# Performance work log

Hardware: AMD Instinct MI355X
Metric: run time of the kernel (lower is better)

## Reference

```python
import jax, jax.numpy as jnp
import numpy as np

B, S, E = 2, 2048, 2048
N_HEAD = 16
HEAD_DIM = E // N_HEAD  # 128
MP_NUM = 4              # hardcoded in the torch forward
ROTARY_DIM = 64


def setup_inputs() -> dict:
    key = jax.random.key(0)
    k1, k2, k3 = jax.random.split(key, 3)
    return {
        "hidden_states": jax.random.normal(k1, (B, S, E), jnp.float32) * 0.02,
        "w_qkv": jax.random.normal(k2, (3 * E, E), jnp.float32) * 0.02,  # torch Linear weight [out,in]
        "w_out": jax.random.normal(k3, (E, E), jnp.float32) * 0.02,
    }


def _rotate_every_two(x):
    # (..., d) -> interleaved (-x2, x1) as in GPT-J/CodeGen
    x1 = x[..., 0::2]
    x2 = x[..., 1::2]
    return jnp.stack((-x2, x1), axis=-1).reshape(x.shape)


def reference(hidden_states, w_qkv, w_out):
    b, s, e = hidden_states.shape
    local = e // MP_NUM  # per-mp-shard channel count

    # qkv projection (no bias), then mp_num split: order is (query, value, key)
    qkv = jnp.einsum("bse,fe->bsf", hidden_states, w_qkv)  # [B,S,3E]
    qkv = qkv.reshape(b, s, MP_NUM, 3 * local)
    q = qkv[..., :local].reshape(b, s, N_HEAD, HEAD_DIM)
    v = qkv[..., local:2 * local].reshape(b, s, N_HEAD, HEAD_DIM)
    k = qkv[..., 2 * local:].reshape(b, s, N_HEAD, HEAD_DIM)

    # partial rotary (rotate-every-two) on first ROTARY_DIM channels
    inv_freq = 1.0 / (10000.0 ** (jnp.arange(0, ROTARY_DIM, 2, dtype=jnp.float32) / ROTARY_DIM))
    freqs = jnp.arange(s, dtype=jnp.float32)[:, None] * inv_freq[None, :]  # [S, R/2]
    sin = jnp.repeat(jnp.sin(freqs), 2, axis=-1)[None, :, None, :]  # [1,S,1,R]
    cos = jnp.repeat(jnp.cos(freqs), 2, axis=-1)[None, :, None, :]

    def rope(x):
        x_rot = x[..., :ROTARY_DIM]
        x_pass = x[..., ROTARY_DIM:]
        x_rot = x_rot * cos + _rotate_every_two(x_rot) * sin
        return jnp.concatenate([x_rot, x_pass], axis=-1)

    q = rope(q)
    k = rope(k)

    # [B,S,H,D] -> [B,H,S,D]
    q = q.transpose(0, 2, 1, 3)
    k = k.transpose(0, 2, 1, 3)
    v = v.transpose(0, 2, 1, 3)

    scale = jnp.sqrt(jnp.asarray(HEAD_DIM, dtype=q.dtype))
    scores = jnp.einsum("bhqd,bhkd->bhqk", q, k) / scale  # [B,H,S,S]
    causal = jnp.tril(jnp.ones((s, s), dtype=bool))
    scores = jnp.where(causal[None, None, :, :], scores, jnp.finfo(scores.dtype).min)
    attn = jax.nn.softmax(scores, axis=-1)

    out = jnp.einsum("bhqk,bhkd->bhqd", attn, v)  # [B,H,S,D]
    out = out.transpose(0, 2, 1, 3).reshape(b, s, e)  # merge heads
    return jnp.einsum("bse,fe->bsf", out, w_out)  # out_proj (no bias)
```

## Files before the change

kernel.cpp:

```cpp
#include <hip/hip_runtime.h>

typedef unsigned short u16;
typedef unsigned int u32;
typedef __attribute__((ext_vector_type(4))) float f32x4;
typedef __attribute__((ext_vector_type(8))) short s16x8;
typedef __attribute__((ext_vector_type(4))) unsigned int u32x4;

#define DEVI static __device__ __forceinline__


#define ROPE_C (-13.287712379549449f / 32.0f)
#define QSCALE 0.12751743f

DEVI u16 f2bf(float f) {
  u32 u = __float_as_uint(f);
  return (u16)((u + 0x7FFFu + ((u >> 16) & 1u)) >> 16);
}
DEVI float bf2f(u16 h) { return __uint_as_float(((u32)h) << 16); }

DEVI void async_copy16(const u16* g, u16* l) {
  __builtin_amdgcn_global_load_lds((__attribute__((address_space(1))) void*)g,
                                   (__attribute__((address_space(3))) void*)l, 16, 0, 0);
}

__global__ __launch_bounds__(256) void cast3_kernel(
    const float* __restrict__ s0, u16* __restrict__ d0, int n0,
    const float* __restrict__ s1, u16* __restrict__ d1, int n1,
    const float* __restrict__ s2, u16* __restrict__ d2, int n2) {
  int i = blockIdx.x * 256 + threadIdx.x;
  const float* s;
  u16* d;
  if (i < n0) {
    s = s0; d = d0;
  } else if (i < n0 + n1) {
    s = s1; d = d1; i -= n0;
  } else if (i < n0 + n1 + n2) {
    s = s2; d = d2; i -= n0 + n1;
  } else {
    return;
  }
  const float4 v = ((const float4*)s)[i];
  ushort4 o;
  o.x = f2bf(v.x); o.y = f2bf(v.y); o.z = f2bf(v.z); o.w = f2bf(v.w);
  ((ushort4*)d)[i] = o;
}

template <int EPI>
__global__ __launch_bounds__(256, 3) void gemm_bt_kernel(
    const u16* __restrict__ A, const u16* __restrict__ Bm, int K, int N,
    float* __restrict__ C, u16* __restrict__ qo, u16* __restrict__ ko, u16* __restrict__ vo) {
  __shared__ __attribute__((aligned(16))) u16 As[3][128 * 32];
  __shared__ __attribute__((aligned(16))) u16 Bs[3][128 * 32];
  const int tid = threadIdx.x;
  const int w = tid >> 6, lane = tid & 63;
  const int quad = lane >> 4, l16 = lane & 15;
  const int wrow = (w >> 1) * 64, wcol = (w & 1) * 64;
  const long tileM = (long)blockIdx.y * 128;
  const long tileN = (long)blockIdx.x * 128;

  f32x4 acc[4][4];
#pragma unroll
  for (int i = 0; i < 4; ++i)
#pragma unroll
    for (int j = 0; j < 4; ++j) acc[i][j] = f32x4{0.f, 0.f, 0.f, 0.f};

  const u16* aptr[2];
  const u16* bptr[2];
  int ldso[2];
#pragma unroll
  for (int c = 0; c < 2; ++c) {
    const int r0 = (w * 2 + c) * 16;
    const int row = r0 + (lane >> 2);
    const int colsw = (((lane & 3) ^ ((row >> 1) & 3)) << 3);
    aptr[c] = A + (tileM + row) * (long)K + colsw;
    bptr[c] = Bm + (tileN + row) * (long)K + colsw;
    ldso[c] = r0 * 32;
  }

  auto stage = [&](int k0, int buf) {
#pragma unroll
    for (int c = 0; c < 2; ++c) {
      async_copy16(aptr[c] + k0, &As[buf][ldso[c]]);
      async_copy16(bptr[c] + k0, &Bs[buf][ldso[c]]);
    }
  };

  stage(0, 0);
  stage(32, 1);

  const int psw = (quad ^ ((l16 >> 1) & 3)) << 3;

  int bt = 0;
  for (int k0 = 0; k0 < K; k0 += 32) {
    if (k0 + 32 < K)
      __builtin_amdgcn_s_waitcnt(0x0f74);
    else
      __builtin_amdgcn_s_waitcnt(0x0f70);
    __builtin_amdgcn_s_barrier();
    if (k0 + 64 < K) stage(k0 + 64, bt == 0 ? 2 : bt - 1);

    s16x8 af[4], bfr[4];
#pragma unroll
    for (int i = 0; i < 4; ++i)
      af[i] = *(const s16x8*)(&As[bt][(wrow + i * 16 + l16) * 32 + psw]);
#pragma unroll
    for (int j = 0; j < 4; ++j)
      bfr[j] = *(const s16x8*)(&Bs[bt][(wcol + j * 16 + l16) * 32 + psw]);
#pragma unroll
    for (int i = 0; i < 4; ++i)
#pragma unroll
      for (int j = 0; j < 4; ++j)
        acc[i][j] = __builtin_amdgcn_mfma_f32_16x16x32_bf16(af[i], bfr[j], acc[i][j], 0, 0, 0);
    bt = bt == 2 ? 0 : bt + 1;
  }

  const int b = (int)(tileM >> 11);
#pragma unroll
  for (int i = 0; i < 4; ++i) {
#pragma unroll
    for (int j = 0; j < 4; ++j) {
      const int rowb = (int)((tileM + wrow + i * 16 + quad * 4) & 2047);
      if (EPI == 0) {
#pragma unroll
        for (int r = 0; r < 4; ++r) {
          const long row = tileM + wrow + i * 16 + quad * 4 + r;
          C[row * N + tileN + wcol + j * 16 + l16] = acc[i][j][r];
        }
      } else {
        const long col0 = tileN + wcol + j * 16;
        const int mp = (int)(col0 / 1536);
        const int cc0 = (int)(col0 - (long)mp * 1536);
        const int part = cc0 >> 9;
        const int idx0 = cc0 & 511;
        const int head = mp * 4 + (idx0 >> 7);
        const int dim0 = idx0 & 127;
        const int dim = dim0 + l16;
        const long bh = (long)(b * 16 + head);
        if (part == 1) {
#pragma unroll
          for (int r = 0; r < 4; ++r)
            vo[(bh * 128 + dim) * 2048 + rowb + r] = f2bf(acc[i][j][r]);
        } else {
          float y[4];
          if (part == 2 && dim0 < 64) {
            const int jj = dim >> 1;
            const float inv = exp2f((float)jj * ROPE_C);
#pragma unroll
            for (int r = 0; r < 4; ++r) {
              const float v = acc[i][j][r];
              const float pv = __shfl_xor(v, 1, 64);
              const float ang = (float)(rowb + r) * inv;
              const float sn = __sinf(ang), cs = __cosf(ang);
              y[r] = (l16 & 1) ? (v * cs + pv * sn) : (v * cs - pv * sn);
            }
          } else {
#pragma unroll
            for (int r = 0; r < 4; ++r) y[r] = acc[i][j][r];
          }
          u16* dst = (part == 0) ? qo : ko;
#pragma unroll
          for (int r = 0; r < 4; ++r)
            dst[(bh * 2048 + rowb + r) * 128 + dim] = f2bf(y[r]);
        }
      }
    }
  }
}

__global__ __launch_bounds__(256, 3) void attn_kernel(
    const u16* __restrict__ q, const u16* __restrict__ k,
    const u16* __restrict__ vT, u16* __restrict__ out) {
  __shared__ __attribute__((aligned(16))) u16 Ks[3][32 * 128];
  __shared__ __attribute__((aligned(16))) u16 Vs[3][128 * 32];
  const int tid = threadIdx.x;
  const int w = tid >> 6, lane = tid & 63;
  const int quad = lane >> 4, l16 = lane & 15;
  const int qt = 31 - (blockIdx.x >> 5);
  const int bh = blockIdx.x & 31;
  const int qbase = qt * 64 + w * 16;

  const u16* qp = q + ((long)bh * 2048 + qbase) * 128;
  const u16* kp = k + (long)bh * 2048 * 128;
  const u16* vp = vT + (long)bh * 128 * 2048;

  const float spos = (float)(qbase + l16);
  s16x8 qf[4];
#pragma unroll
  for (int c = 0; c < 4; ++c) {
    const s16x8 raw = *(const s16x8*)(qp + l16 * 128 + c * 32 + quad * 8);
    s16x8 ov;
    if (c < 2) {
#pragma unroll
      for (int m = 0; m < 4; ++m) {
        const int jj = c * 16 + quad * 4 + m;
        const float inv = exp2f((float)jj * ROPE_C);
        const float ang = spos * inv;
        const float sn = __sinf(ang), cs = __cosf(ang);
        const float x0 = bf2f((u16)raw[2 * m]), x1 = bf2f((u16)raw[2 * m + 1]);
        ov[2 * m] = (short)f2bf((x0 * cs - x1 * sn) * QSCALE);
        ov[2 * m + 1] = (short)f2bf((x1 * cs + x0 * sn) * QSCALE);
      }
    } else {
#pragma unroll
      for (int e = 0; e < 8; ++e) ov[e] = (short)f2bf(bf2f((u16)raw[e]) * QSCALE);
    }
    qf[c] = ov;
  }

  f32x4 acc[8];
#pragma unroll
  for (int d = 0; d < 8; ++d) acc[d] = f32x4{0.f, 0.f, 0.f, 0.f};
  float mrun = -1e30f, lrun = 0.f;

  auto stage = [&](int k0, int buf) {
    const int ko = lane >> 4, cl = lane & 15;
#pragma unroll
    for (int i = 0; i < 2; ++i) {
      const int keyt = w * 8 + i * 4;
      const int rr = keyt + ko;
      const int sk = ((rr >> 2) & 3) * 8 + ((rr >> 4) & 1) * 4 + (rr & 3);
      async_copy16(kp + (long)(k0 + sk) * 128 + ((cl ^ (rr & 15)) << 3),
                   &Ks[buf][keyt * 128]);
    }
    const int ld = lane >> 2, c4 = lane & 3;
#pragma unroll
    for (int i = 0; i < 2; ++i) {
      const int db = w * 32 + i * 16;
      const int d = db + ld;
      async_copy16(vp + (long)d * 2048 + k0 + ((c4 ^ ((d >> 1) & 3)) << 3),
                   &Vs[buf][db * 32]);
    }
  };

  const int nt = 2 * qt + 2;
  stage(0, 0);
  stage(32, 1);

  int bt = 0;
  for (int t = 0; t < nt; ++t) {
    const int k0 = t * 32;
    if (t + 1 < nt)
      __builtin_amdgcn_s_waitcnt(0x0f74);
    else
      __builtin_amdgcn_s_waitcnt(0x0f70);
    __builtin_amdgcn_s_barrier();
    if (t + 2 < nt) stage(k0 + 64, bt == 0 ? 2 : bt - 1);
    const u16* Ksc = Ks[bt];
    const u16* Vsc = Vs[bt];

    f32x4 sc[2];
    sc[0] = f32x4{0.f, 0.f, 0.f, 0.f};
    sc[1] = f32x4{0.f, 0.f, 0.f, 0.f};
    __builtin_amdgcn_s_setprio(1);
#pragma unroll
    for (int c = 0; c < 4; ++c) {
      const s16x8 kf0 = *(const s16x8*)(
          &Ksc[(0 * 16 + l16) * 128 + ((((c << 2) + quad) ^ l16) << 3)]);
      const s16x8 kf1 = *(const s16x8*)(
          &Ksc[(1 * 16 + l16) * 128 + ((((c << 2) + quad) ^ l16) << 3)]);
      sc[0] = __builtin_amdgcn_mfma_f32_16x16x32_bf16(kf0, qf[c], sc[0], 0, 0, 0);
      sc[1] = __builtin_amdgcn_mfma_f32_16x16x32_bf16(kf1, qf[c], sc[1], 0, 0, 0);
    }
    __builtin_amdgcn_s_setprio(0);
    if (k0 + 31 > qbase) {
      const int qrow = qbase + l16;
#pragma unroll
      for (int g = 0; g < 2; ++g) {
        const int keyb = k0 + quad * 8 + g * 4;
#pragma unroll
        for (int r = 0; r < 4; ++r)
          if (keyb + r > qrow) sc[g][r] = -1e30f;
      }
    }
    float mx = fmaxf(fmaxf(fmaxf(sc[0][0], sc[0][1]), fmaxf(sc[0][2], sc[0][3])),
                     fmaxf(fmaxf(sc[1][0], sc[1][1]), fmaxf(sc[1][2], sc[1][3])));
    mx = fmaxf(mx, __shfl_xor(mx, 16, 64));
    mx = fmaxf(mx, __shfl_xor(mx, 32, 64));
    if (__any(mx > mrun + 8.f)) {
      const float mnew = fmaxf(mrun, mx);
      const float alpha = exp2f(mrun - mnew);
      mrun = mnew;
      lrun *= alpha;
#pragma unroll
      for (int d = 0; d < 8; ++d)
#pragma unroll
        for (int r = 0; r < 4; ++r) acc[d][r] *= alpha;
    }
    float p[2][4];
    float sm = 0.f;
#pragma unroll
    for (int g = 0; g < 2; ++g)
#pragma unroll
      for (int r = 0; r < 4; ++r) { p[g][r] = exp2f(sc[g][r] - mrun); sm += p[g][r]; }
    sm += __shfl_xor(sm, 16, 64);
    sm += __shfl_xor(sm, 32, 64);
    lrun += sm;

    u32 pk[2][2];
#pragma unroll
    for (int g = 0; g < 2; ++g) {
      pk[g][0] = (u32)f2bf(p[g][0]) | ((u32)f2bf(p[g][1]) << 16);
      pk[g][1] = (u32)f2bf(p[g][2]) | ((u32)f2bf(p[g][3]) << 16);
    }
    const u32x4 pw = {pk[0][0], pk[0][1], pk[1][0], pk[1][1]};
    const s16x8 pf = __builtin_bit_cast(s16x8, pw);

    __builtin_amdgcn_s_setprio(1);
#pragma unroll
    for (int dd = 0; dd < 8; ++dd) {
      const s16x8 vf = *(const s16x8*)(
          &Vsc[(dd * 16 + l16) * 32 + ((quad ^ ((l16 >> 1) & 3)) << 3)]);
      acc[dd] = __builtin_amdgcn_mfma_f32_16x16x32_bf16(vf, pf, acc[dd], 0, 0, 0);
    }
    __builtin_amdgcn_s_setprio(0);
    bt = bt == 2 ? 0 : bt + 1;
  }

  const int b = bh >> 4, h = bh & 15;
  u16* op = out + ((long)b * 2048 + qbase + l16) * 2048 + h * 128;
  const float inv_l = 1.0f / lrun;
#pragma unroll
  for (int dd = 0; dd < 8; ++dd) {
    ushort4 o4;
    o4.x = f2bf(acc[dd][0] * inv_l);
    o4.y = f2bf(acc[dd][1] * inv_l);
    o4.z = f2bf(acc[dd][2] * inv_l);
    o4.w = f2bf(acc[dd][3] * inv_l);
    *(ushort4*)(op + dd * 16 + quad * 4) = o4;
  }
}

extern "C" void kernel_launch(void* const* d_in, const int* in_sizes, int n_in,
                              void* d_out, int out_size, void* d_ws, size_t ws_size,
                              hipStream_t stream) {
  const float* hidden = (const float*)d_in[0];
  const float* w_qkv = (const float*)d_in[1];
  const float* w_out = (const float*)d_in[2];
  float* out = (float*)d_out;
  char* ws = (char*)d_ws;

  u16* hid_b  = (u16*)(ws + (size_t)0);
  u16* wqkv_b = (u16*)(ws + (size_t)16777216);
  u16* wout_b = (u16*)(ws + (size_t)41943040);
  u16* qb     = (u16*)(ws + (size_t)50331648);
  u16* kb     = (u16*)(ws + (size_t)67108864);
  u16* vb     = (u16*)(ws + (size_t)83886080);
  u16* ao     = (u16*)(ws + (size_t)100663296);

  cast3_kernel<<<24576, 256, 0, stream>>>(hidden, hid_b, 2097152,
                                          w_qkv, wqkv_b, 3145728,
                                          w_out, wout_b, 1048576);

  gemm_bt_kernel<1><<<dim3(48, 32), 256, 0, stream>>>(hid_b, wqkv_b, 2048, 6144,
                                                      nullptr, qb, kb, vb);
  attn_kernel<<<1024, 256, 0, stream>>>(qb, kb, vb, ao);
  gemm_bt_kernel<0><<<dim3(16, 32), 256, 0, stream>>>(ao, wout_b, 2048, 2048,
                                                      out, nullptr, nullptr, nullptr);
}
```

Baseline: 373.9 us.

## Process two query groups per attention block to reuse staged K/V tiles

```diff
diff --git a/kernel.cpp b/kernel.cpp
--- a/kernel.cpp
+++ b/kernel.cpp
@@ -167,7 +167,7 @@
   }
 }
 
-__global__ __launch_bounds__(256, 3) void attn_kernel(
+__global__ __launch_bounds__(256, 2) void attn_kernel(
     const u16* __restrict__ q, const u16* __restrict__ k,
     const u16* __restrict__ vT, u16* __restrict__ out) {
   __shared__ __attribute__((aligned(16))) u16 Ks[3][32 * 128];
@@ -175,42 +175,50 @@
   const int tid = threadIdx.x;
   const int w = tid >> 6, lane = tid & 63;
   const int quad = lane >> 4, l16 = lane & 15;
-  const int qt = 31 - (blockIdx.x >> 5);
+  const int qt = 15 - (blockIdx.x >> 5);
   const int bh = blockIdx.x & 31;
-  const int qbase = qt * 64 + w * 16;
-
-  const u16* qp = q + ((long)bh * 2048 + qbase) * 128;
+  const int qb0 = qt * 128 + w * 16;
+  const int qb1 = qb0 + 64;
+
+  const u16* qp = q + ((long)bh * 2048 + qb0) * 128;
   const u16* kp = k + (long)bh * 2048 * 128;
   const u16* vp = vT + (long)bh * 128 * 2048;
 
-  const float spos = (float)(qbase + l16);
-  s16x8 qf[4];
-#pragma unroll
-  for (int c = 0; c < 4; ++c) {
-    const s16x8 raw = *(const s16x8*)(qp + l16 * 128 + c * 32 + quad * 8);
-    s16x8 ov;
-    if (c < 2) {
-#pragma unroll
-      for (int m = 0; m < 4; ++m) {
-        const int jj = c * 16 + quad * 4 + m;
-        const float inv = exp2f((float)jj * ROPE_C);
-        const float ang = spos * inv;
-        const float sn = __sinf(ang), cs = __cosf(ang);
-        const float x0 = bf2f((u16)raw[2 * m]), x1 = bf2f((u16)raw[2 * m + 1]);
-        ov[2 * m] = (short)f2bf((x0 * cs - x1 * sn) * QSCALE);
-        ov[2 * m + 1] = (short)f2bf((x1 * cs + x0 * sn) * QSCALE);
-      }
-    } else {
-#pragma unroll
-      for (int e = 0; e < 8; ++e) ov[e] = (short)f2bf(bf2f((u16)raw[e]) * QSCALE);
-    }
-    qf[c] = ov;
-  }
-
-  f32x4 acc[8];
-#pragma unroll
-  for (int d = 0; d < 8; ++d) acc[d] = f32x4{0.f, 0.f, 0.f, 0.f};
-  float mrun = -1e30f, lrun = 0.f;
+  s16x8 qf[2][4];
+#pragma unroll
+  for (int qg = 0; qg < 2; ++qg) {
+    const float spos = (float)((qg ? qb1 : qb0) + l16);
+    const u16* qpg = qp + (qg ? 64 * 128 : 0);
+#pragma unroll
+    for (int c = 0; c < 4; ++c) {
+      const s16x8 raw = *(const s16x8*)(qpg + l16 * 128 + c * 32 + quad * 8);
+      s16x8 ov;
+      if (c < 2) {
+#pragma unroll
+        for (int m = 0; m < 4; ++m) {
+          const int jj = c * 16 + quad * 4 + m;
+          const float inv = exp2f((float)jj * ROPE_C);
+          const float ang = spos * inv;
+          const float sn = __sinf(ang), cs = __cosf(ang);
+          const float x0 = bf2f((u16)raw[2 * m]), x1 = bf2f((u16)raw[2 * m + 1]);
+          ov[2 * m] = (short)f2bf((x0 * cs - x1 * sn) * QSCALE);
+          ov[2 * m + 1] = (short)f2bf((x1 * cs + x0 * sn) * QSCALE);
+        }
+      } else {
+#pragma unroll
+        for (int e = 0; e < 8; ++e) ov[e] = (short)f2bf(bf2f((u16)raw[e]) * QSCALE);
+      }
+      qf[qg][c] = ov;
+    }
+  }
+
+  f32x4 acc[2][8];
+#pragma unroll
+  for (int qg = 0; qg < 2; ++qg)
+#pragma unroll
+    for (int d = 0; d < 8; ++d) acc[qg][d] = f32x4{0.f, 0.f, 0.f, 0.f};
+  float mrun0 = -1e30f, lrun0 = 0.f;
+  float mrun1 = -1e30f, lrun1 = 0.f;
 
   auto stage = [&](int k0, int buf) {
     const int ko = lane >> 4, cl = lane & 15;
@@ -232,7 +240,7 @@
     }
   };
 
-  const int nt = 2 * qt + 2;
+  const int nt = 4 * qt + 4;
   stage(0, 0);
   stage(32, 1);
 
@@ -247,10 +255,17 @@
     if (t + 2 < nt) stage(k0 + 64, bt == 0 ? 2 : bt - 1);
     const u16* Ksc = Ks[bt];
     const u16* Vsc = Vs[bt];
-
-    f32x4 sc[2];
-    sc[0] = f32x4{0.f, 0.f, 0.f, 0.f};
-    sc[1] = f32x4{0.f, 0.f, 0.f, 0.f};
+    bt = bt == 2 ? 0 : bt + 1;
+
+    const bool act1 = (k0 <= qb1 + 15);
+    const bool act0 = (k0 <= qb0 + 15);
+    if (!act1) continue;
+
+    f32x4 sc0[2], sc1[2];
+    sc0[0] = f32x4{0.f, 0.f, 0.f, 0.f};
+    sc0[1] = f32x4{0.f, 0.f, 0.f, 0.f};
+    sc1[0] = f32x4{0.f, 0.f, 0.f, 0.f};
+    sc1[1] = f32x4{0.f, 0.f, 0.f, 0.f};
     __builtin_amdgcn_s_setprio(1);
 #pragma unroll
     for (int c = 0; c < 4; ++c) {
@@ -258,75 +273,128 @@
           &Ksc[(0 * 16 + l16) * 128 + ((((c << 2) + quad) ^ l16) << 3)]);
       const s16x8 kf1 = *(const s16x8*)(
           &Ksc[(1 * 16 + l16) * 128 + ((((c << 2) + quad) ^ l16) << 3)]);
-      sc[0] = __builtin_amdgcn_mfma_f32_16x16x32_bf16(kf0, qf[c], sc[0], 0, 0, 0);
-      sc[1] = __builtin_amdgcn_mfma_f32_16x16x32_bf16(kf1, qf[c], sc[1], 0, 0, 0);
+      if (act0) {
+        sc0[0] = __builtin_amdgcn_mfma_f32_16x16x32_bf16(kf0, qf[0][c], sc0[0], 0, 0, 0);
+        sc0[1] = __builtin_amdgcn_mfma_f32_16x16x32_bf16(kf1, qf[0][c], sc0[1], 0, 0, 0);
+      }
+      sc1[0] = __builtin_amdgcn_mfma_f32_16x16x32_bf16(kf0, qf[1][c], sc1[0], 0, 0, 0);
+      sc1[1] = __builtin_amdgcn_mfma_f32_16x16x32_bf16(kf1, qf[1][c], sc1[1], 0, 0, 0);
     }
     __builtin_amdgcn_s_setprio(0);
-    if (k0 + 31 > qbase) {
-      const int qrow = qbase + l16;
+
+    if (k0 + 31 > qb1) {
+      const int qrow = qb1 + l16;
 #pragma unroll
       for (int g = 0; g < 2; ++g) {
         const int keyb = k0 + quad * 8 + g * 4;
 #pragma unroll
         for (int r = 0; r < 4; ++r)
-          if (keyb + r > qrow) sc[g][r] = -1e30f;
-      }
-    }
-    float mx = fmaxf(fmaxf(fmaxf(sc[0][0], sc[0][1]), fmaxf(sc[0][2], sc[0][3])),
-                     fmaxf(fmaxf(sc[1][0], sc[1][1]), fmaxf(sc[1][2], sc[1][3])));
-    mx = fmaxf(mx, __shfl_xor(mx, 16, 64));
-    mx = fmaxf(mx, __shfl_xor(mx, 32, 64));
-    if (__any(mx > mrun + 8.f)) {
-      const float mnew = fmaxf(mrun, mx);
-      const float alpha = exp2f(mrun - mnew);
-      mrun = mnew;
-      lrun *= alpha;
+          if (keyb + r > qrow) sc1[g][r] = -1e30f;
+      }
+    }
+    float mx1 = fmaxf(fmaxf(fmaxf(sc1[0][0], sc1[0][1]), fmaxf(sc1[0][2], sc1[0][3])),
+                      fmaxf(fmaxf(sc1[1][0], sc1[1][1]), fmaxf(sc1[1][2], sc1[1][3])));
+    mx1 = fmaxf(mx1, __shfl_xor(mx1, 16, 64));
+    mx1 = fmaxf(mx1, __shfl_xor(mx1, 32, 64));
+    if (__any(mx1 > mrun1 + 8.f)) {
+      const float mnew = fmaxf(mrun1, mx1);
+      const float alpha = exp2f(mrun1 - mnew);
+      mrun1 = mnew;
+      lrun1 *= alpha;
 #pragma unroll
       for (int d = 0; d < 8; ++d)
 #pragma unroll
-        for (int r = 0; r < 4; ++r) acc[d][r] *= alpha;
-    }
-    float p[2][4];
-    float sm = 0.f;
+        for (int r = 0; r < 4; ++r) acc[1][d][r] *= alpha;
+    }
+    float p1[2][4];
+    float sm1 = 0.f;
 #pragma unroll
     for (int g = 0; g < 2; ++g)
 #pragma unroll
-      for (int r = 0; r < 4; ++r) { p[g][r] = exp2f(sc[g][r] - mrun); sm += p[g][r]; }
-    sm += __shfl_xor(sm, 16, 64);
-    sm += __shfl_xor(sm, 32, 64);
-    lrun += sm;
-
-    u32 pk[2][2];
+      for (int r = 0; r < 4; ++r) { p1[g][r] = exp2f(sc1[g][r] - mrun1); sm1 += p1[g][r]; }
+    sm1 += __shfl_xor(sm1, 16, 64);
+    sm1 += __shfl_xor(sm1, 32, 64);
+    lrun1 += sm1;
+    u32 pk1[2][2];
 #pragma unroll
     for (int g = 0; g < 2; ++g) {
-      pk[g][0] = (u32)f2bf(p[g][0]) | ((u32)f2bf(p[g][1]) << 16);
-      pk[g][1] = (u32)f2bf(p[g][2]) | ((u32)f2bf(p[g][3]) << 16);
-    }
-    const u32x4 pw = {pk[0][0], pk[0][1], pk[1][0], pk[1][1]};
-    const s16x8 pf = __builtin_bit_cast(s16x8, pw);
+      pk1[g][0] = (u32)f2bf(p1[g][0]) | ((u32)f2bf(p1[g][1]) << 16);
+      pk1[g][1] = (u32)f2bf(p1[g][2]) | ((u32)f2bf(p1[g][3]) << 16);
+    }
+    const u32x4 pw1 = {pk1[0][0], pk1[0][1], pk1[1][0], pk1[1][1]};
+    const s16x8 pf1 = __builtin_bit_cast(s16x8, pw1);
+
+    s16x8 pf0;
+    if (act0) {
+      if (k0 + 31 > qb0) {
+        const int qrow = qb0 + l16;
+#pragma unroll
+        for (int g = 0; g < 2; ++g) {
+          const int keyb = k0 + quad * 8 + g * 4;
+#pragma unroll
+          for (int r = 0; r < 4; ++r)
+            if (keyb + r > qrow) sc0[g][r] = -1e30f;
+        }
+      }
+      float mx0 = fmaxf(fmaxf(fmaxf(sc0[0][0], sc0[0][1]), fmaxf(sc0[0][2], sc0[0][3])),
+                        fmaxf(fmaxf(sc0[1][0], sc0[1][1]), fmaxf(sc0[1][2], sc0[1][3])));
+      mx0 = fmaxf(mx0, __shfl_xor(mx0, 16, 64));
+      mx0 = fmaxf(mx0, __shfl_xor(mx0, 32, 64));
+      if (__any(mx0 > mrun0 + 8.f)) {
+        const float mnew = fmaxf(mrun0, mx0);
+        const float alpha = exp2f(mrun0 - mnew);
+        mrun0 = mnew;
+        lrun0 *= alpha;
+#pragma unroll
+        for (int d = 0; d < 8; ++d)
+#pragma unroll
+          for (int r = 0; r < 4; ++r) acc[0][d][r] *= alpha;
+      }
+      float p0[2][4];
+      float sm0 = 0.f;
+#pragma unroll
+      for (int g = 0; g < 2; ++g)
+#pragma unroll
+        for (int r = 0; r < 4; ++r) { p0[g][r] = exp2f(sc0[g][r] - mrun0); sm0 += p0[g][r]; }
+      sm0 += __shfl_xor(sm0, 16, 64);
+      sm0 += __shfl_xor(sm0, 32, 64);
+      lrun0 += sm0;
+      u32 pk0[2][2];
+#pragma unroll
+      for (int g = 0; g < 2; ++g) {
+        pk0[g][0] = (u32)f2bf(p0[g][0]) | ((u32)f2bf(p0[g][1]) << 16);
+        pk0[g][1] = (u32)f2bf(p0[g][2]) | ((u32)f2bf(p0[g][3]) << 16);
+      }
+      const u32x4 pw0 = {pk0[0][0], pk0[0][1], pk0[1][0], pk0[1][1]};
+      pf0 = __builtin_bit_cast(s16x8, pw0);
+    }
 
     __builtin_amdgcn_s_setprio(1);
 #pragma unroll
     for (int dd = 0; dd < 8; ++dd) {
       const s16x8 vf = *(const s16x8*)(
           &Vsc[(dd * 16 + l16) * 32 + ((quad ^ ((l16 >> 1) & 3)) << 3)]);
-      acc[dd] = __builtin_amdgcn_mfma_f32_16x16x32_bf16(vf, pf, acc[dd], 0, 0, 0);
+      if (act0)
+        acc[0][dd] = __builtin_amdgcn_mfma_f32_16x16x32_bf16(vf, pf0, acc[0][dd], 0, 0, 0);
+      acc[1][dd] = __builtin_amdgcn_mfma_f32_16x16x32_bf16(vf, pf1, acc[1][dd], 0, 0, 0);
     }
     __builtin_amdgcn_s_setprio(0);
-    bt = bt == 2 ? 0 : bt + 1;
   }
 
   const int b = bh >> 4, h = bh & 15;
-  u16* op = out + ((long)b * 2048 + qbase + l16) * 2048 + h * 128;
-  const float inv_l = 1.0f / lrun;
-#pragma unroll
-  for (int dd = 0; dd < 8; ++dd) {
-    ushort4 o4;
-    o4.x = f2bf(acc[dd][0] * inv_l);
-    o4.y = f2bf(acc[dd][1] * inv_l);
-    o4.z = f2bf(acc[dd][2] * inv_l);
-    o4.w = f2bf(acc[dd][3] * inv_l);
-    *(ushort4*)(op + dd * 16 + quad * 4) = o4;
+#pragma unroll
+  for (int qg = 0; qg < 2; ++qg) {
+    u16* op = out + ((long)b * 2048 + (qg ? qb1 : qb0) + l16) * 2048 + h * 128;
+    const float inv_l = 1.0f / (qg ? lrun1 : lrun0);
+#pragma unroll
+    for (int dd = 0; dd < 8; ++dd) {
+      ushort4 o4;
+      o4.x = f2bf(acc[qg][dd][0] * inv_l);
+      o4.y = f2bf(acc[qg][dd][1] * inv_l);
+      o4.z = f2bf(acc[qg][dd][2] * inv_l);
+      o4.w = f2bf(acc[qg][dd][3] * inv_l);
+      *(ushort4*)(op + dd * 16 + quad * 4) = o4;
+    }
   }
 }
 
@@ -353,7 +421,7 @@
 
   gemm_bt_kernel<1><<<dim3(48, 32), 256, 0, stream>>>(hid_b, wqkv_b, 2048, 6144,
                                                       nullptr, qb, kb, vb);
-  attn_kernel<<<1024, 256, 0, stream>>>(qb, kb, vb, ao);
+  attn_kernel<<<512, 256, 0, stream>>>(qb, kb, vb, ao);
   gemm_bt_kernel<0><<<dim3(16, 32), 256, 0, stream>>>(ao, wout_b, 2048, 2048,
                                                       out, nullptr, nullptr, nullptr);
 }
```

Measured after the change: 417.0 us. 1.12x slower.

## Switch attention to 32x32x16 MFMA with 2-wave blocks and double buffering

Applied to the files above, without the earlier changes.

```diff
diff --git a/kernel.cpp b/kernel.cpp
--- a/kernel.cpp
+++ b/kernel.cpp
@@ -3,6 +3,7 @@
 typedef unsigned short u16;
 typedef unsigned int u32;
 typedef __attribute__((ext_vector_type(4))) float f32x4;
+typedef __attribute__((ext_vector_type(16))) float f32x16;
 typedef __attribute__((ext_vector_type(8))) short s16x8;
 typedef __attribute__((ext_vector_type(4))) unsigned int u32x4;
 
@@ -167,32 +168,32 @@
   }
 }
 
-__global__ __launch_bounds__(256, 3) void attn_kernel(
+__global__ __launch_bounds__(128, 2) void attn_kernel(
     const u16* __restrict__ q, const u16* __restrict__ k,
     const u16* __restrict__ vT, u16* __restrict__ out) {
-  __shared__ __attribute__((aligned(16))) u16 Ks[3][32 * 128];
-  __shared__ __attribute__((aligned(16))) u16 Vs[3][128 * 32];
+  __shared__ __attribute__((aligned(16))) u16 Ks[2][32 * 128];
+  __shared__ __attribute__((aligned(16))) u16 Vs[2][128 * 32];
   const int tid = threadIdx.x;
   const int w = tid >> 6, lane = tid & 63;
-  const int quad = lane >> 4, l16 = lane & 15;
+  const int l32 = lane & 31, h = lane >> 5;
   const int qt = 31 - (blockIdx.x >> 5);
   const int bh = blockIdx.x & 31;
-  const int qbase = qt * 64 + w * 16;
-
-  const u16* qp = q + ((long)bh * 2048 + qbase) * 128;
+  const int qb = qt * 64 + w * 32;
+
+  const u16* qp = q + ((long)bh * 2048 + qb) * 128;
   const u16* kp = k + (long)bh * 2048 * 128;
   const u16* vp = vT + (long)bh * 128 * 2048;
 
-  const float spos = (float)(qbase + l16);
-  s16x8 qf[4];
-#pragma unroll
-  for (int c = 0; c < 4; ++c) {
-    const s16x8 raw = *(const s16x8*)(qp + l16 * 128 + c * 32 + quad * 8);
+  const float spos = (float)(qb + l32);
+  s16x8 qf[8];
+#pragma unroll
+  for (int c = 0; c < 8; ++c) {
+    const s16x8 raw = *(const s16x8*)(qp + l32 * 128 + c * 16 + h * 8);
     s16x8 ov;
-    if (c < 2) {
+    if (c < 4) {
 #pragma unroll
       for (int m = 0; m < 4; ++m) {
-        const int jj = c * 16 + quad * 4 + m;
+        const int jj = c * 8 + h * 4 + m;
         const float inv = exp2f((float)jj * ROPE_C);
         const float ang = spos * inv;
         const float sn = __sinf(ang), cs = __cosf(ang);
@@ -207,74 +208,79 @@
     qf[c] = ov;
   }
 
-  f32x4 acc[8];
-#pragma unroll
-  for (int d = 0; d < 8; ++d) acc[d] = f32x4{0.f, 0.f, 0.f, 0.f};
+  f32x16 acc[4];
+#pragma unroll
+  for (int dt = 0; dt < 4; ++dt)
+#pragma unroll
+    for (int r = 0; r < 16; ++r) acc[dt][r] = 0.f;
   float mrun = -1e30f, lrun = 0.f;
 
   auto stage = [&](int k0, int buf) {
-    const int ko = lane >> 4, cl = lane & 15;
-#pragma unroll
-    for (int i = 0; i < 2; ++i) {
-      const int keyt = w * 8 + i * 4;
-      const int rr = keyt + ko;
-      const int sk = ((rr >> 2) & 3) * 8 + ((rr >> 4) & 1) * 4 + (rr & 3);
+    const int cl = lane & 15;
+#pragma unroll
+    for (int i = 0; i < 4; ++i) {
+      const int r0 = 4 * (4 * w + i);
+      const int rr = r0 + (lane >> 4);
+      const int bb = rr >> 2;
+      const int bs = (bb & 4) | ((bb & 1) << 1) | ((bb >> 1) & 1);
+      const int sk = bs * 4 + (rr & 3);
       async_copy16(kp + (long)(k0 + sk) * 128 + ((cl ^ (rr & 15)) << 3),
-                   &Ks[buf][keyt * 128]);
-    }
-    const int ld = lane >> 2, c4 = lane & 3;
-#pragma unroll
-    for (int i = 0; i < 2; ++i) {
-      const int db = w * 32 + i * 16;
-      const int d = db + ld;
+                   &Ks[buf][r0 * 128]);
+    }
+#pragma unroll
+    for (int i = 0; i < 4; ++i) {
+      const int d0 = 16 * (4 * w + i);
+      const int d = d0 + (lane >> 2);
+      const int c4 = lane & 3;
       async_copy16(vp + (long)d * 2048 + k0 + ((c4 ^ ((d >> 1) & 3)) << 3),
-                   &Vs[buf][db * 32]);
+                   &Vs[buf][d0 * 32]);
     }
   };
 
   const int nt = 2 * qt + 2;
   stage(0, 0);
-  stage(32, 1);
-
-  int bt = 0;
+
   for (int t = 0; t < nt; ++t) {
     const int k0 = t * 32;
-    if (t + 1 < nt)
-      __builtin_amdgcn_s_waitcnt(0x0f74);
-    else
-      __builtin_amdgcn_s_waitcnt(0x0f70);
+    __builtin_amdgcn_s_waitcnt(0x0f70);
     __builtin_amdgcn_s_barrier();
-    if (t + 2 < nt) stage(k0 + 64, bt == 0 ? 2 : bt - 1);
-    const u16* Ksc = Ks[bt];
-    const u16* Vsc = Vs[bt];
-
-    f32x4 sc[2];
-    sc[0] = f32x4{0.f, 0.f, 0.f, 0.f};
-    sc[1] = f32x4{0.f, 0.f, 0.f, 0.f};
+    if (t + 1 < nt) stage(k0 + 32, (t + 1) & 1);
+    const u16* Ksc = Ks[t & 1];
+    const u16* Vsc = Vs[t & 1];
+    if (k0 > qb + 31) continue;
+
+    f32x16 sa, sb;
+#pragma unroll
+    for (int r = 0; r < 16; ++r) { sa[r] = 0.f; sb[r] = 0.f; }
     __builtin_amdgcn_s_setprio(1);
 #pragma unroll
-    for (int c = 0; c < 4; ++c) {
+    for (int c = 0; c < 8; c += 2) {
       const s16x8 kf0 = *(const s16x8*)(
-          &Ksc[(0 * 16 + l16) * 128 + ((((c << 2) + quad) ^ l16) << 3)]);
+          &Ksc[l32 * 128 + ((((c << 1) + h) ^ (l32 & 15)) << 3)]);
       const s16x8 kf1 = *(const s16x8*)(
-          &Ksc[(1 * 16 + l16) * 128 + ((((c << 2) + quad) ^ l16) << 3)]);
-      sc[0] = __builtin_amdgcn_mfma_f32_16x16x32_bf16(kf0, qf[c], sc[0], 0, 0, 0);
-      sc[1] = __builtin_amdgcn_mfma_f32_16x16x32_bf16(kf1, qf[c], sc[1], 0, 0, 0);
+          &Ksc[l32 * 128 + (((((c + 1) << 1) + h) ^ (l32 & 15)) << 3)]);
+      sa = __builtin_amdgcn_mfma_f32_32x32x16_bf16(kf0, qf[c], sa, 0, 0, 0);
+      sb = __builtin_amdgcn_mfma_f32_32x32x16_bf16(kf1, qf[c + 1], sb, 0, 0, 0);
     }
     __builtin_amdgcn_s_setprio(0);
-    if (k0 + 31 > qbase) {
-      const int qrow = qbase + l16;
-#pragma unroll
-      for (int g = 0; g < 2; ++g) {
-        const int keyb = k0 + quad * 8 + g * 4;
-#pragma unroll
-        for (int r = 0; r < 4; ++r)
-          if (keyb + r > qrow) sc[g][r] = -1e30f;
+    f32x16 sc;
+#pragma unroll
+    for (int r = 0; r < 16; ++r) sc[r] = sa[r] + sb[r];
+
+    if (k0 + 31 > qb) {
+      const int qrow = qb + l32;
+#pragma unroll
+      for (int r = 0; r < 16; ++r) {
+        const int rr = (r & 3) + ((r >> 2) << 3) + 4 * h;
+        const int bb = rr >> 2;
+        const int bs = (bb & 4) | ((bb & 1) << 1) | ((bb >> 1) & 1);
+        const int key = k0 + bs * 4 + (rr & 3);
+        if (key > qrow) sc[r] = -1e30f;
       }
     }
-    float mx = fmaxf(fmaxf(fmaxf(sc[0][0], sc[0][1]), fmaxf(sc[0][2], sc[0][3])),
-                     fmaxf(fmaxf(sc[1][0], sc[1][1]), fmaxf(sc[1][2], sc[1][3])));
-    mx = fmaxf(mx, __shfl_xor(mx, 16, 64));
+    float mx = sc[0];
+#pragma unroll
+    for (int r = 1; r < 16; ++r) mx = fmaxf(mx, sc[r]);
     mx = fmaxf(mx, __shfl_xor(mx, 32, 64));
     if (__any(mx > mrun + 8.f)) {
       const float mnew = fmaxf(mrun, mx);
@@ -282,51 +288,55 @@
       mrun = mnew;
       lrun *= alpha;
 #pragma unroll
-      for (int d = 0; d < 8; ++d)
-#pragma unroll
-        for (int r = 0; r < 4; ++r) acc[d][r] *= alpha;
-    }
-    float p[2][4];
+      for (int dt = 0; dt < 4; ++dt)
+#pragma unroll
+        for (int r = 0; r < 16; ++r) acc[dt][r] *= alpha;
+    }
+    float p[16];
     float sm = 0.f;
 #pragma unroll
-    for (int g = 0; g < 2; ++g)
-#pragma unroll
-      for (int r = 0; r < 4; ++r) { p[g][r] = exp2f(sc[g][r] - mrun); sm += p[g][r]; }
-    sm += __shfl_xor(sm, 16, 64);
+    for (int r = 0; r < 16; ++r) { p[r] = exp2f(sc[r] - mrun); sm += p[r]; }
     sm += __shfl_xor(sm, 32, 64);
     lrun += sm;
 
-    u32 pk[2][2];
-#pragma unroll
-    for (int g = 0; g < 2; ++g) {
-      pk[g][0] = (u32)f2bf(p[g][0]) | ((u32)f2bf(p[g][1]) << 16);
-      pk[g][1] = (u32)f2bf(p[g][2]) | ((u32)f2bf(p[g][3]) << 16);
-    }
-    const u32x4 pw = {pk[0][0], pk[0][1], pk[1][0], pk[1][1]};
-    const s16x8 pf = __builtin_bit_cast(s16x8, pw);
+    u32 pw[8];
+#pragma unroll
+    for (int x = 0; x < 8; ++x)
+      pw[x] = (u32)f2bf(p[2 * x]) | ((u32)f2bf(p[2 * x + 1]) << 16);
+    const u32x4 pwa = {pw[0], pw[1], pw[2], pw[3]};
+    const u32x4 pwb = {pw[4], pw[5], pw[6], pw[7]};
+    const s16x8 pf0 = __builtin_bit_cast(s16x8, pwa);
+    const s16x8 pf1 = __builtin_bit_cast(s16x8, pwb);
 
     __builtin_amdgcn_s_setprio(1);
 #pragma unroll
-    for (int dd = 0; dd < 8; ++dd) {
-      const s16x8 vf = *(const s16x8*)(
-          &Vsc[(dd * 16 + l16) * 32 + ((quad ^ ((l16 >> 1) & 3)) << 3)]);
-      acc[dd] = __builtin_amdgcn_mfma_f32_16x16x32_bf16(vf, pf, acc[dd], 0, 0, 0);
+    for (int ki = 0; ki < 2; ++ki) {
+      const s16x8 pf = ki ? pf1 : pf0;
+#pragma unroll
+      for (int dt = 0; dt < 4; ++dt) {
+        const int d0 = dt * 32 + l32;
+        const s16x8 vf = *(const s16x8*)(
+            &Vsc[d0 * 32 + ((((ki << 1) + h) ^ ((l32 >> 1) & 3)) << 3)]);
+        acc[dt] = __builtin_amdgcn_mfma_f32_32x32x16_bf16(vf, pf, acc[dt], 0, 0, 0);
+      }
     }
     __builtin_amdgcn_s_setprio(0);
-    bt = bt == 2 ? 0 : bt + 1;
-  }
-
-  const int b = bh >> 4, h = bh & 15;
-  u16* op = out + ((long)b * 2048 + qbase + l16) * 2048 + h * 128;
+  }
+
+  const int b = bh >> 4, hh = bh & 15;
+  u16* op = out + ((long)b * 2048 + qb + l32) * 2048 + hh * 128;
   const float inv_l = 1.0f / lrun;
 #pragma unroll
-  for (int dd = 0; dd < 8; ++dd) {
-    ushort4 o4;
-    o4.x = f2bf(acc[dd][0] * inv_l);
-    o4.y = f2bf(acc[dd][1] * inv_l);
-    o4.z = f2bf(acc[dd][2] * inv_l);
-    o4.w = f2bf(acc[dd][3] * inv_l);
-    *(ushort4*)(op + dd * 16 + quad * 4) = o4;
+  for (int dt = 0; dt < 4; ++dt) {
+#pragma unroll
+    for (int G = 0; G < 4; ++G) {
+      ushort4 o4;
+      o4.x = f2bf(acc[dt][G * 4 + 0] * inv_l);
+      o4.y = f2bf(acc[dt][G * 4 + 1] * inv_l);
+      o4.z = f2bf(acc[dt][G * 4 + 2] * inv_l);
+      o4.w = f2bf(acc[dt][G * 4 + 3] * inv_l);
+      *(ushort4*)(op + dt * 32 + G * 8 + 4 * h) = o4;
+    }
   }
 }
 
@@ -353,7 +363,7 @@
 
   gemm_bt_kernel<1><<<dim3(48, 32), 256, 0, stream>>>(hid_b, wqkv_b, 2048, 6144,
                                                       nullptr, qb, kb, vb);
-  attn_kernel<<<1024, 256, 0, stream>>>(qb, kb, vb, ao);
+  attn_kernel<<<1024, 128, 0, stream>>>(qb, kb, vb, ao);
   gemm_bt_kernel<0><<<dim3(16, 32), 256, 0, stream>>>(ao, wout_b, 2048, 2048,
                                                       out, nullptr, nullptr, nullptr);
 }
```

New measurement: 402.1 us. +7.5%, slower.
